# Kernel tuning notes

Measured on AMD Instinct MI355X. Metric: run time of the kernel, lower is better.

Reference implementation:

```python
import jax, jax.numpy as jnp
import numpy as np

NUM_FREQS = 10
EPS = 1e-6


def _posenc(x):
    # NeRF positional encoding with identity: [x, sin(2^i x), cos(2^i x)]
    freqs = 2.0 ** jnp.arange(NUM_FREQS, dtype=x.dtype)  # [L]
    xb = x[..., None, :] * freqs[:, None]                # [..., L, D]
    four = jnp.sin(jnp.concatenate([xb, xb + 0.5 * jnp.pi], axis=-2))
    return jnp.concatenate([x, four.reshape(*x.shape[:-1], -1)], axis=-1)


def _ln(x, s, b):
    mu = jnp.mean(x, axis=-1, keepdims=True)
    var = jnp.mean(jnp.square(x - mu), axis=-1, keepdims=True)
    return (x - mu) * jax.lax.rsqrt(var + EPS) * s + b


def _layer(net, chunk, hW, hb, hls, hlb, wW, wb, bW, bb_, ls, lb):
    # hyper net (hyper_depth=1): Dense -> LayerNorm -> relu
    h = jax.nn.relu(_ln(chunk @ hW + hb, hls, hlb))
    n_in = net.shape[-1]
    n_out = bb_.shape[-1]
    # generate per-point weight matrix [K,P,N,M] and bias [K,P,N]
    w = (h @ wW + wb).reshape(*h.shape[:-1], n_out, n_in)
    b = h @ bW + bb_
    net = jnp.einsum('kpm,kpnm->kpn', net, w) + b
    return jax.nn.relu(_ln(net, ls, lb))


def _forward(rays, latent_tokens, token_embeddings, h_W0, h_b0, h_ln_s0, h_ln_b0,
             w_W0, w_b0, bb_W0, bb_b0, ln_s0, ln_b0,
             h_W, h_b, h_ln_s, h_ln_b, w_W, w_b, bb_W, bb_b, ln_s, ln_b,
             rgb_W, rgb_b):
    origins = rays[..., 0:3]
    dirs = rays[..., 3:6]
    plucker = jnp.concatenate([dirs, jnp.cross(origins, dirs)], axis=-1)  # [K,P,6]
    net = _posenc(plucker)  # [K,P,126]

    K, T, Z = latent_tokens.shape
    emb = jnp.broadcast_to(token_embeddings[None], (K, T, token_embeddings.shape[-1]))
    lt = jnp.concatenate([latent_tokens, emb], axis=-1).reshape(K, 1, -1)  # [K,1,T*(Z+E)]
    P = rays.shape[1]
    latent = jnp.broadcast_to(lt, (K, P, lt.shape[-1]))
    skips = jnp.split(latent, 8, axis=-1)  # 8 chunks of [K,P,128]

    net = _layer(net, skips[0], h_W0, h_b0, h_ln_s0, h_ln_b0,
                 w_W0, w_b0, bb_W0, bb_b0, ln_s0, ln_b0)
    for i in range(7):
        net = _layer(net, skips[i + 1], h_W[i], h_b[i], h_ln_s[i], h_ln_b[i],
                     w_W[i], w_b[i], bb_W[i], bb_b[i], ln_s[i], ln_b[i])
    return jax.nn.sigmoid(net @ rgb_W + rgb_b)


def setup_inputs() -> dict:
    key = jax.random.key(0)
    ks = jax.random.split(key, 12)
    K, P, T, Z, W = 2, 4096, 8, 64, 64
    IN0 = 6 * (1 + 2 * NUM_FREQS)  # 126
    f32 = jnp.float32
    d = {}
    d['rays'] = jax.random.normal(ks[0], (K, P, 6), f32)
    d['latent_tokens'] = jax.random.normal(ks[1], (K, T, Z), f32)
    d['token_embeddings'] = jax.random.normal(ks[2], (T, 64), f32)
    # layer 0 (input dim 126)
    d['h_W0'] = jax.random.normal(ks[3], (Z + 64, W), f32)
    d['h_b0'] = jnp.zeros((W,), f32)
    d['h_ln_s0'] = jnp.ones((W,), f32)
    d['h_ln_b0'] = jnp.zeros((W,), f32)
    d['w_W0'] = jax.random.normal(ks[4], (W, IN0 * W), f32)
    d['w_b0'] = jnp.zeros((IN0 * W,), f32)
    d['bb_W0'] = jax.random.normal(ks[5], (W, W), f32)
    d['bb_b0'] = jnp.zeros((W,), f32)
    d['ln_s0'] = jnp.ones((W,), f32)
    d['ln_b0'] = jnp.zeros((W,), f32)
    # layers 1..7 (input dim 64), stacked
    L = 7
    d['h_W'] = jax.random.normal(ks[6], (L, Z + 64, W), f32)
    d['h_b'] = jnp.zeros((L, W), f32)
    d['h_ln_s'] = jnp.ones((L, W), f32)
    d['h_ln_b'] = jnp.zeros((L, W), f32)
    d['w_W'] = jax.random.normal(ks[7], (L, W, W * W), f32)
    d['w_b'] = jnp.zeros((L, W * W), f32)
    d['bb_W'] = jax.random.normal(ks[8], (L, W, W), f32)
    d['bb_b'] = jnp.zeros((L, W), f32)
    d['ln_s'] = jnp.ones((L, W), f32)
    d['ln_b'] = jnp.zeros((L, W), f32)
    d['rgb_W'] = jax.random.normal(ks[9], (W, 3), f32)
    d['rgb_b'] = jnp.zeros((3,), f32)
    return d


def reference(rays, latent_tokens, token_embeddings, h_W0, h_b0, h_ln_s0, h_ln_b0,
              w_W0, w_b0, bb_W0, bb_b0, ln_s0, ln_b0,
              h_W, h_b, h_ln_s, h_ln_b, w_W, w_b, bb_W, bb_b, ln_s, ln_b,
              rgb_W, rgb_b):
    return _forward(rays, latent_tokens, token_embeddings, h_W0, h_b0, h_ln_s0, h_ln_b0,
                    w_W0, w_b0, bb_W0, bb_b0, ln_s0, ln_b0,
                    h_W, h_b, h_ln_s, h_ln_b, w_W, w_b, bb_W, bb_b, ln_s, ln_b,
                    rgb_W, rgb_b)
```

## Files before the change

kernel.cpp:

```cpp
#include <hip/hip_runtime.h>
#include <math.h>

#define EPSF 1e-6f
#define RPW 4

__device__ __forceinline__ float rl(float v, int srclane) {
    return __uint_as_float(__builtin_amdgcn_readlane(__float_as_uint(v), srclane));
}

__device__ __forceinline__ float wave_sum64(float v) {
#pragma unroll
    for (int off = 32; off > 0; off >>= 1) v += __shfl_xor(v, off, 64);
    return v;
}

__device__ __forceinline__ void ln_stats(float a, float& mu, float& rstd) {
    float s1 = a, s2 = a * a;
#pragma unroll
    for (int off = 32; off > 0; off >>= 1) {
        s1 += __shfl_xor(s1, off, 64);
        s2 += __shfl_xor(s2, off, 64);
    }
    mu = s1 * (1.0f / 64.0f);
    float var = fmaxf(s2 * (1.0f / 64.0f) - mu * mu, 0.0f);
    rstd = rsqrtf(var + EPSF);
}

__device__ __forceinline__ float posenc_elem(const float* pl, int e) {
    if (e < 6) return pl[e];
    int t = e - 6;
    int j = t / 6;
    int i = t - j * 6;
    int jm = (j < 10) ? j : (j - 10);
    float arg = pl[i] * (float)(1 << jm);
    if (j >= 10) arg += 1.5707963705062866f;
    return sinf(arg);
}

__global__ __launch_bounds__(128, 4) void precompute_kernel(
    const float* __restrict__ latent_tokens, const float* __restrict__ token_embeddings,
    const float* __restrict__ h_W0, const float* __restrict__ h_b0,
    const float* __restrict__ h_ln_s0, const float* __restrict__ h_ln_b0,
    const float* __restrict__ w_W0, const float* __restrict__ w_b0,
    const float* __restrict__ bb_W0, const float* __restrict__ bb_b0,
    const float* __restrict__ h_W, const float* __restrict__ h_b,
    const float* __restrict__ h_ln_s, const float* __restrict__ h_ln_b,
    const float* __restrict__ w_W, const float* __restrict__ w_b,
    const float* __restrict__ bb_W, const float* __restrict__ bb_b,
    float* __restrict__ ws, int offW, int offB)
{
    const int s = blockIdx.x;
    const int l = blockIdx.y;
    const int k = blockIdx.z;
    const int tid = threadIdx.x;

    __shared__ float s_chunk[128];
    __shared__ float s_h[64];

    s_chunk[tid] = (tid < 64) ? latent_tokens[(k * 8 + l) * 64 + tid]
                              : token_embeddings[l * 64 + (tid - 64)];
    __syncthreads();

    const float* hW  = (l == 0) ? h_W0    : h_W    + (size_t)(l - 1) * 128 * 64;
    const float* hb  = (l == 0) ? h_b0    : h_b    + (l - 1) * 64;
    const float* hls = (l == 0) ? h_ln_s0 : h_ln_s + (l - 1) * 64;
    const float* hlb = (l == 0) ? h_ln_b0 : h_ln_b + (l - 1) * 64;

    if (tid < 64) {
        float acc = hb[tid];
#pragma unroll 16
        for (int m = 0; m < 128; m++) acc += s_chunk[m] * hW[m * 64 + tid];
        float mu, rstd;
        ln_stats(acc, mu, rstd);
        float y = (acc - mu) * rstd * hls[tid] + hlb[tid];
        s_h[tid] = fmaxf(y, 0.0f);
    }
    __syncthreads();

    const int n_in  = (l == 0) ? 126 : 64;
    const int nflat = 64 * n_in;
    const int slice = nflat / 32;
    const int o0 = s * slice;
    const float* wW = (l == 0) ? w_W0 : w_W + (size_t)(l - 1) * 64 * 4096;
    const float* wb = (l == 0) ? w_b0 : w_b + (size_t)(l - 1) * 4096;
    float* Wt = (l == 0) ? ws + (size_t)k * 8192
                         : ws + offW + ((size_t)k * 7 + (l - 1)) * 4096;

    for (int o = o0 + tid; o < o0 + slice; o += 128) {
        float acc = wb[o];
#pragma unroll 16
        for (int j = 0; j < 64; j++) acc += s_h[j] * wW[j * nflat + o];
        if (l == 0) {
            int n = o / 126;
            int m = o - n * 126;
            Wt[n * 128 + m] = acc;
        } else {
            Wt[o] = acc;
        }
    }

    if (l == 0 && s == 0) {
        Wt[(tid >> 1) * 128 + 126 + (tid & 1)] = 0.0f;
    }

    if (s == 0 && tid < 64) {
        const float* bW  = (l == 0) ? bb_W0 : bb_W + (size_t)(l - 1) * 64 * 64;
        const float* bb_ = (l == 0) ? bb_b0 : bb_b + (l - 1) * 64;
        float acc = bb_[tid];
#pragma unroll 16
        for (int j = 0; j < 64; j++) acc += s_h[j] * bW[j * 64 + tid];
        ws[offB + (k * 8 + l) * 64 + tid] = acc;
    }
}

__global__ __launch_bounds__(256, 3) void forward_kernel(
    const float* __restrict__ rays,
    const float* __restrict__ ln_s0, const float* __restrict__ ln_b0,
    const float* __restrict__ ln_s, const float* __restrict__ ln_b,
    const float* __restrict__ rgb_W, const float* __restrict__ rgb_b,
    const float* __restrict__ ws, int offW, int offB,
    float* __restrict__ out, int K, int P)
{
    const int warp = threadIdx.x >> 6;
    const int lane = threadIdx.x & 63;
    const int total = K * P;
    const int r0 = (blockIdx.x * 4 + warp) * RPW;
    if (r0 >= total) return;
    const int k = r0 / P;

    float net0[RPW], net1[RPW];
#pragma unroll
    for (int q = 0; q < RPW; q++) {
        int r = r0 + q; if (r > total - 1) r = total - 1;
        float o0 = rays[r * 6 + 0], o1 = rays[r * 6 + 1], o2 = rays[r * 6 + 2];
        float d0 = rays[r * 6 + 3], d1 = rays[r * 6 + 4], d2 = rays[r * 6 + 5];
        float pl[6];
        pl[0] = d0; pl[1] = d1; pl[2] = d2;
        pl[3] = o1 * d2 - o2 * d1;
        pl[4] = o2 * d0 - o0 * d2;
        pl[5] = o0 * d1 - o1 * d0;
        net0[q] = posenc_elem(pl, lane);
        net1[q] = (lane + 64 < 126) ? posenc_elem(pl, lane + 64) : 0.0f;
    }

    const float* WL = ws + offW + (size_t)k * 7 * 4096;
    float acc[RPW];
    float4 w4[16];

    {
        const float4* row = (const float4*)(ws + (size_t)k * 8192 + lane * 128);
        float4 w4b[16];
#pragma unroll
        for (int j = 0; j < 16; j++) w4[j]  = row[j];
#pragma unroll
        for (int j = 0; j < 16; j++) w4b[j] = row[16 + j];
        float bia = ws[offB + (k * 8 + 0) * 64 + lane];
        float pre[RPW];
#pragma unroll
        for (int q = 0; q < RPW; q++) pre[q] = bia;
#pragma unroll
        for (int m = 0; m < 64; m++) {
            float wm = ((const float*)w4)[m];
#pragma unroll
            for (int q = 0; q < RPW; q++) pre[q] += rl(net0[q], m) * wm;
        }
#pragma unroll
        for (int m = 0; m < 64; m++) {
            float wm = ((const float*)w4b)[m];
#pragma unroll
            for (int q = 0; q < RPW; q++) pre[q] += rl(net1[q], m) * wm;
        }
        const float4* nrow = (const float4*)(WL + lane * 64);
#pragma unroll
        for (int j = 0; j < 16; j++) w4[j] = nrow[j];
        float s = ln_s0[lane], b = ln_b0[lane];
#pragma unroll
        for (int q = 0; q < RPW; q++) {
            float mu, rstd;
            ln_stats(pre[q], mu, rstd);
            acc[q] = fmaxf((pre[q] - mu) * rstd * s + b, 0.0f);
        }
    }

#pragma unroll 1
    for (int l = 1; l < 8; l++) {
        float na[RPW];
        float bia = ws[offB + (k * 8 + l) * 64 + lane];
#pragma unroll
        for (int q = 0; q < RPW; q++) na[q] = bia;
#pragma unroll
        for (int m = 0; m < 64; m++) {
            float wm = ((const float*)w4)[m];
#pragma unroll
            for (int q = 0; q < RPW; q++) na[q] += rl(acc[q], m) * wm;
        }
        {
            int lp = (l < 7) ? l : 6;
            const float4* nrow = (const float4*)(WL + (size_t)lp * 4096 + lane * 64);
#pragma unroll
            for (int j = 0; j < 16; j++) w4[j] = nrow[j];
        }
        float s = ln_s[(l - 1) * 64 + lane], b = ln_b[(l - 1) * 64 + lane];
#pragma unroll
        for (int q = 0; q < RPW; q++) {
            float mu, rstd;
            ln_stats(na[q], mu, rstd);
            acc[q] = fmaxf((na[q] - mu) * rstd * s + b, 0.0f);
        }
    }

    float w0 = rgb_W[lane * 3 + 0], w1 = rgb_W[lane * 3 + 1], w2 = rgb_W[lane * 3 + 2];
    float b0 = rgb_b[0], b1 = rgb_b[1], b2 = rgb_b[2];
#pragma unroll
    for (int q = 0; q < RPW; q++) {
        float c0 = wave_sum64(acc[q] * w0);
        float c1 = wave_sum64(acc[q] * w1);
        float c2 = wave_sum64(acc[q] * w2);
        if (lane == 0 && r0 + q < total) {
            out[(r0 + q) * 3 + 0] = 1.0f / (1.0f + expf(-(c0 + b0)));
            out[(r0 + q) * 3 + 1] = 1.0f / (1.0f + expf(-(c1 + b1)));
            out[(r0 + q) * 3 + 2] = 1.0f / (1.0f + expf(-(c2 + b2)));
        }
    }
}

extern "C" void kernel_launch(void* const* d_in, const int* in_sizes, int n_in,
                              void* d_out, int out_size, void* d_ws, size_t ws_size,
                              hipStream_t stream) {
    const float* rays    = (const float*)d_in[0];
    const float* latent  = (const float*)d_in[1];
    const float* tok_emb = (const float*)d_in[2];
    const float* h_W0    = (const float*)d_in[3];
    const float* h_b0    = (const float*)d_in[4];
    const float* h_ln_s0 = (const float*)d_in[5];
    const float* h_ln_b0 = (const float*)d_in[6];
    const float* w_W0    = (const float*)d_in[7];
    const float* w_b0    = (const float*)d_in[8];
    const float* bb_W0   = (const float*)d_in[9];
    const float* bb_b0   = (const float*)d_in[10];
    const float* ln_s0   = (const float*)d_in[11];
    const float* ln_b0   = (const float*)d_in[12];
    const float* h_W     = (const float*)d_in[13];
    const float* h_b     = (const float*)d_in[14];
    const float* h_ln_s  = (const float*)d_in[15];
    const float* h_ln_b  = (const float*)d_in[16];
    const float* w_W     = (const float*)d_in[17];
    const float* w_b     = (const float*)d_in[18];
    const float* bb_W    = (const float*)d_in[19];
    const float* bb_b    = (const float*)d_in[20];
    const float* ln_s    = (const float*)d_in[21];
    const float* ln_b    = (const float*)d_in[22];
    const float* rgb_W   = (const float*)d_in[23];
    const float* rgb_b   = (const float*)d_in[24];
    float* out = (float*)d_out;

    const int K = in_sizes[1] / (8 * 64);
    const int P = in_sizes[0] / (6 * K);
    const int offW = K * 8192;
    const int offB = offW + K * 7 * 4096;

    float* ws = (float*)d_ws;

    dim3 pgrid(32, 8, K);
    precompute_kernel<<<pgrid, 128, 0, stream>>>(
        latent, tok_emb, h_W0, h_b0, h_ln_s0, h_ln_b0, w_W0, w_b0, bb_W0, bb_b0,
        h_W, h_b, h_ln_s, h_ln_b, w_W, w_b, bb_W, bb_b, ws, offW, offB);

    const int total = K * P;
    const int rays_per_block = 4 * RPW;
    const int blocks = (total + rays_per_block - 1) / rays_per_block;
    forward_kernel<<<blocks, 256, 0, stream>>>(
        rays, ln_s0, ln_b0, ln_s, ln_b, rgb_W, rgb_b,
        ws, offW, offB, out, K, P);
}
```

Before: 157.0 us.

## Stage per-layer weights in LDS with prefetch pipeline; share weight reads across batches

The forward kernel now stages the generated per-point weight matrices in shared memory, stored transposed as [m][n]. It double-buffers the next layer's weights through registers and a ring of LDS slots, so each lane no longer holds a full weight row in 64 registers. The precompute kernel now processes both batch items in one block, so every w_W element is loaded once and used for two outputs. The trade-offs are 64KB of LDS per block, which limits occupancy, plus extra __syncthreads. The code also hardcodes K=2 and drops the early-exit bounds check.

```diff
diff --git a/kernel.cpp b/kernel.cpp
--- a/kernel.cpp
+++ b/kernel.cpp
@@ -6,12 +6,6 @@
 
 __device__ __forceinline__ float rl(float v, int srclane) {
     return __uint_as_float(__builtin_amdgcn_readlane(__float_as_uint(v), srclane));
-}
-
-__device__ __forceinline__ float wave_sum64(float v) {
-#pragma unroll
-    for (int off = 32; off > 0; off >>= 1) v += __shfl_xor(v, off, 64);
-    return v;
 }
 
 __device__ __forceinline__ void ln_stats(float a, float& mu, float& rstd) {
@@ -24,6 +18,12 @@
     mu = s1 * (1.0f / 64.0f);
     float var = fmaxf(s2 * (1.0f / 64.0f) - mu * mu, 0.0f);
     rstd = rsqrtf(var + EPSF);
+}
+
+__device__ __forceinline__ float wave_sum64(float v) {
+#pragma unroll
+    for (int off = 32; off > 0; off >>= 1) v += __shfl_xor(v, off, 64);
+    return v;
 }
 
 __device__ __forceinline__ float posenc_elem(const float* pl, int e) {
@@ -37,7 +37,7 @@
     return sinf(arg);
 }
 
-__global__ __launch_bounds__(128, 4) void precompute_kernel(
+__global__ __launch_bounds__(128) void precompute_kernel(
     const float* __restrict__ latent_tokens, const float* __restrict__ token_embeddings,
     const float* __restrict__ h_W0, const float* __restrict__ h_b0,
     const float* __restrict__ h_ln_s0, const float* __restrict__ h_ln_b0,
@@ -51,14 +51,19 @@
 {
     const int s = blockIdx.x;
     const int l = blockIdx.y;
-    const int k = blockIdx.z;
     const int tid = threadIdx.x;
-
-    __shared__ float s_chunk[128];
-    __shared__ float s_h[64];
-
-    s_chunk[tid] = (tid < 64) ? latent_tokens[(k * 8 + l) * 64 + tid]
-                              : token_embeddings[l * 64 + (tid - 64)];
+    const int lane = tid & 63;
+    const int warp = tid >> 6;
+
+    __shared__ float s_chunk[2][128];
+    __shared__ float s_h[2][64];
+
+#pragma unroll
+    for (int t = tid; t < 256; t += 128) {
+        int k = t >> 7, m = t & 127;
+        s_chunk[k][m] = (m < 64) ? latent_tokens[(k * 8 + l) * 64 + m]
+                                 : token_embeddings[l * 64 + (m - 64)];
+    }
     __syncthreads();
 
     const float* hW  = (l == 0) ? h_W0    : h_W    + (size_t)(l - 1) * 128 * 64;
@@ -66,54 +71,58 @@
     const float* hls = (l == 0) ? h_ln_s0 : h_ln_s + (l - 1) * 64;
     const float* hlb = (l == 0) ? h_ln_b0 : h_ln_b + (l - 1) * 64;
 
-    if (tid < 64) {
-        float acc = hb[tid];
+    {
+        float a = hb[lane];
 #pragma unroll 16
-        for (int m = 0; m < 128; m++) acc += s_chunk[m] * hW[m * 64 + tid];
+        for (int m = 0; m < 128; m++) a += s_chunk[warp][m] * hW[m * 64 + lane];
         float mu, rstd;
-        ln_stats(acc, mu, rstd);
-        float y = (acc - mu) * rstd * hls[tid] + hlb[tid];
-        s_h[tid] = fmaxf(y, 0.0f);
+        ln_stats(a, mu, rstd);
+        s_h[warp][lane] = fmaxf((a - mu) * rstd * hls[lane] + hlb[lane], 0.0f);
     }
     __syncthreads();
 
     const int n_in  = (l == 0) ? 126 : 64;
     const int nflat = 64 * n_in;
     const int slice = nflat / 32;
-    const int o0 = s * slice;
     const float* wW = (l == 0) ? w_W0 : w_W + (size_t)(l - 1) * 64 * 4096;
     const float* wb = (l == 0) ? w_b0 : w_b + (size_t)(l - 1) * 4096;
-    float* Wt = (l == 0) ? ws + (size_t)k * 8192
-                         : ws + offW + ((size_t)k * 7 + (l - 1)) * 4096;
-
-    for (int o = o0 + tid; o < o0 + slice; o += 128) {
-        float acc = wb[o];
+
+    for (int o = s * slice + tid; o < s * slice + slice; o += 128) {
+        float wbv = wb[o];
+        float a0 = wbv, a1 = wbv;
 #pragma unroll 16
-        for (int j = 0; j < 64; j++) acc += s_h[j] * wW[j * nflat + o];
+        for (int j = 0; j < 64; j++) {
+            float w = wW[(size_t)j * nflat + o];
+            a0 += s_h[0][j] * w;
+            a1 += s_h[1][j] * w;
+        }
+        int n = o / n_in, m = o - n * n_in;
         if (l == 0) {
-            int n = o / 126;
-            int m = o - n * 126;
-            Wt[n * 128 + m] = acc;
+            ws[m * 64 + n] = a0;
+            ws[8192 + m * 64 + n] = a1;
         } else {
-            Wt[o] = acc;
+            float* base = ws + offW + (size_t)(l - 1) * 4096;
+            base[m * 64 + n] = a0;
+            base[7 * 4096 + m * 64 + n] = a1;
         }
     }
 
     if (l == 0 && s == 0) {
-        Wt[(tid >> 1) * 128 + 126 + (tid & 1)] = 0.0f;
-    }
-
-    if (s == 0 && tid < 64) {
+        ws[8064 + tid] = 0.0f;
+        ws[8192 + 8064 + tid] = 0.0f;
+    }
+
+    if (s == 0) {
         const float* bW  = (l == 0) ? bb_W0 : bb_W + (size_t)(l - 1) * 64 * 64;
         const float* bb_ = (l == 0) ? bb_b0 : bb_b + (l - 1) * 64;
-        float acc = bb_[tid];
+        float a = bb_[lane];
 #pragma unroll 16
-        for (int j = 0; j < 64; j++) acc += s_h[j] * bW[j * 64 + tid];
-        ws[offB + (k * 8 + l) * 64 + tid] = acc;
-    }
-}
-
-__global__ __launch_bounds__(256, 3) void forward_kernel(
+        for (int j = 0; j < 64; j++) a += s_h[warp][j] * bW[j * 64 + lane];
+        ws[offB + (warp * 8 + l) * 64 + lane] = a;
+    }
+}
+
+__global__ __launch_bounds__(256) void forward_kernel(
     const float* __restrict__ rays,
     const float* __restrict__ ln_s0, const float* __restrict__ ln_b0,
     const float* __restrict__ ln_s, const float* __restrict__ ln_b,
@@ -121,12 +130,23 @@
     const float* __restrict__ ws, int offW, int offB,
     float* __restrict__ out, int K, int P)
 {
-    const int warp = threadIdx.x >> 6;
-    const int lane = threadIdx.x & 63;
+    __shared__ float Lds[16384];
+    const int tid  = threadIdx.x;
+    const int warp = tid >> 6;
+    const int lane = tid & 63;
     const int total = K * P;
-    const int r0 = (blockIdx.x * 4 + warp) * RPW;
-    if (r0 >= total) return;
-    const int k = r0 / P;
+    const int base = blockIdx.x * (4 * RPW);
+    const int k = base / P;
+    const int r0 = base + warp * RPW;
+
+    const float4* gW0 = (const float4*)(ws + (size_t)k * 8192);
+    const float4* gWL = (const float4*)(ws + offW + (size_t)k * 7 * 4096);
+
+    float4 pf[4];
+#pragma unroll
+    for (int it = 0; it < 4; it++) pf[it] = gWL[tid + it * 256];
+#pragma unroll
+    for (int it = 0; it < 8; it++) ((float4*)Lds)[tid + it * 256] = gW0[tid + it * 256];
 
     float net0[RPW], net1[RPW];
 #pragma unroll
@@ -143,69 +163,68 @@
         net1[q] = (lane + 64 < 126) ? posenc_elem(pl, lane + 64) : 0.0f;
     }
 
-    const float* WL = ws + offW + (size_t)k * 7 * 4096;
+#pragma unroll
+    for (int it = 0; it < 4; it++) ((float4*)(Lds + 2 * 4096))[tid + it * 256] = pf[it];
+#pragma unroll
+    for (int it = 0; it < 4; it++) pf[it] = gWL[1024 + tid + it * 256];
+    __syncthreads();
+
     float acc[RPW];
-    float4 w4[16];
-
     {
-        const float4* row = (const float4*)(ws + (size_t)k * 8192 + lane * 128);
-        float4 w4b[16];
-#pragma unroll
-        for (int j = 0; j < 16; j++) w4[j]  = row[j];
-#pragma unroll
-        for (int j = 0; j < 16; j++) w4b[j] = row[16 + j];
         float bia = ws[offB + (k * 8 + 0) * 64 + lane];
         float pre[RPW];
 #pragma unroll
         for (int q = 0; q < RPW; q++) pre[q] = bia;
 #pragma unroll
         for (int m = 0; m < 64; m++) {
-            float wm = ((const float*)w4)[m];
-#pragma unroll
-            for (int q = 0; q < RPW; q++) pre[q] += rl(net0[q], m) * wm;
+            float wv = Lds[m * 64 + lane];
+#pragma unroll
+            for (int q = 0; q < RPW; q++) pre[q] += rl(net0[q], m) * wv;
         }
 #pragma unroll
         for (int m = 0; m < 64; m++) {
-            float wm = ((const float*)w4b)[m];
-#pragma unroll
-            for (int q = 0; q < RPW; q++) pre[q] += rl(net1[q], m) * wm;
-        }
-        const float4* nrow = (const float4*)(WL + lane * 64);
-#pragma unroll
-        for (int j = 0; j < 16; j++) w4[j] = nrow[j];
-        float s = ln_s0[lane], b = ln_b0[lane];
+            float wv = Lds[(m + 64) * 64 + lane];
+#pragma unroll
+            for (int q = 0; q < RPW; q++) pre[q] += rl(net1[q], m) * wv;
+        }
+        float sc = ln_s0[lane], bc = ln_b0[lane];
 #pragma unroll
         for (int q = 0; q < RPW; q++) {
             float mu, rstd;
             ln_stats(pre[q], mu, rstd);
-            acc[q] = fmaxf((pre[q] - mu) * rstd * s + b, 0.0f);
+            acc[q] = fmaxf((pre[q] - mu) * rstd * sc + bc, 0.0f);
         }
     }
 
 #pragma unroll 1
     for (int l = 1; l < 8; l++) {
+        if (l < 7) {
+            float* dst = Lds + (size_t)(((l + 2) & 3)) * 4096;
+#pragma unroll
+            for (int it = 0; it < 4; it++) ((float4*)dst)[tid + it * 256] = pf[it];
+            if (l < 6) {
+#pragma unroll
+                for (int it = 0; it < 4; it++) pf[it] = gWL[(size_t)(l + 1) * 1024 + tid + it * 256];
+            }
+        }
+        __syncthreads();
+        const float* B = Lds + (size_t)((l + 1) & 3) * 4096;
+        float bia = ws[offB + (k * 8 + l) * 64 + lane];
         float na[RPW];
-        float bia = ws[offB + (k * 8 + l) * 64 + lane];
 #pragma unroll
         for (int q = 0; q < RPW; q++) na[q] = bia;
 #pragma unroll
         for (int m = 0; m < 64; m++) {
-            float wm = ((const float*)w4)[m];
-#pragma unroll
-            for (int q = 0; q < RPW; q++) na[q] += rl(acc[q], m) * wm;
-        }
-        {
-            int lp = (l < 7) ? l : 6;
-            const float4* nrow = (const float4*)(WL + (size_t)lp * 4096 + lane * 64);
-#pragma unroll
-            for (int j = 0; j < 16; j++) w4[j] = nrow[j];
-        }
-        float s = ln_s[(l - 1) * 64 + lane], b = ln_b[(l - 1) * 64 + lane];
+            float wv = B[m * 64 + lane];
+#pragma unroll
+            for (int q = 0; q < RPW; q++) na[q] += rl(acc[q], m) * wv;
+        }
+        float sc = ln_s[(l - 1) * 64 + lane], bc = ln_b[(l - 1) * 64 + lane];
 #pragma unroll
         for (int q = 0; q < RPW; q++) {
             float mu, rstd;
             ln_stats(na[q], mu, rstd);
-            acc[q] = fmaxf((na[q] - mu) * rstd * s + b, 0.0f);
+            acc[q] = fmaxf((na[q] - mu) * rstd * sc + bc, 0.0f);
         }
     }
 
@@ -261,7 +280,7 @@
 
     float* ws = (float*)d_ws;
 
-    dim3 pgrid(32, 8, K);
+    dim3 pgrid(32, 8);
     precompute_kernel<<<pgrid, 128, 0, stream>>>(
         latent, tok_emb, h_W0, h_b0, h_ln_s0, h_ln_b0, w_W0, w_b0, bb_W0, bb_b0,
         h_W, h_b, h_ln_s, h_ln_b, w_W, w_b, bb_W, bb_b, ws, offW, offB);
```

Result: slower. 165.6 us (+5.5%).
